# Optimization experiments

Hardware: AMD Instinct MI355X
Metric: run time of the kernel (lower is better)

Reference implementation:

```python
import jax, jax.numpy as jnp
import numpy as np

H = 16      # heads
D = 64      # head_dim
C = 64      # k_centroid
HID = H * D
TAU1 = 1.0
TAU2 = 1.0


def setup_inputs() -> dict:
    key = jax.random.key(0)
    ks = jax.random.split(key, 12)
    B, S = 4, 1024
    inv = 1.0 / np.sqrt(D)
    return {
        "query": jax.random.normal(ks[0], (B, S, HID), dtype=jnp.float32),
        "key": jax.random.normal(ks[1], (B, S, HID), dtype=jnp.float32),
        "value": jax.random.normal(ks[2], (B, S, HID), dtype=jnp.float32),
        "Wq": jax.random.uniform(ks[3], (D, D), jnp.float32, -inv, inv),
        "bq": jax.random.uniform(ks[4], (D,), jnp.float32, -inv, inv),
        "Wk": jax.random.uniform(ks[5], (D, D), jnp.float32, -inv, inv),
        "bk": jax.random.uniform(ks[6], (D,), jnp.float32, -inv, inv),
        "Wv": jax.random.uniform(ks[7], (D, D), jnp.float32, -inv, inv),
        "bv": jax.random.uniform(ks[8], (D,), jnp.float32, -inv, inv),
        "centroid": jax.random.uniform(ks[9], (D, C), jnp.float32, -0.5, 0.5),
        "Wfc": jax.random.uniform(ks[10], (HID, HID), jnp.float32, -1.0 / np.sqrt(HID), 1.0 / np.sqrt(HID)),
        "bfc": jax.random.uniform(ks[11], (HID,), jnp.float32, -1.0 / np.sqrt(HID), 1.0 / np.sqrt(HID)),
    }


def _forward(query, key, value, Wq, bq, Wk, bk, Wv, bv, centroid, Wfc, bfc):
    B, S, _ = query.shape
    q = query.reshape(B, S, H, D)
    k = key.reshape(B, S, H, D)
    v = value.reshape(B, S, H, D)
    # per-head linear projections (applied on last dim, nn.Linear equivalent)
    Q = jnp.einsum('nshd,de->nshe', q, Wq) + bq
    K = jnp.einsum('nshd,de->nshe', k, Wk) + bk
    V = jnp.einsum('nshd,de->nshe', v, Wv) + bv
    # VQ-style key quantization: project keys onto centroids, gumbel-softmax over codebook
    K_ = jnp.einsum('nshd,dc->nshc', K, centroid)            # [B,S,H,C]
    g1 = jax.random.gumbel(jax.random.key(42), K_.shape, dtype=K_.dtype)
    prob = jax.nn.softmax((K_ + g1) / TAU1, axis=-1)
    sto_K = jnp.einsum('nshc,dc->nshd', prob, centroid)      # prob @ centroid.T
    # gumbel-softmax attention over QK^T
    scores = jnp.einsum('nqhd,nkhd->nhqk', Q, sto_K)         # [B,H,S,S]
    g2 = jax.random.gumbel(jax.random.key(43), scores.shape, dtype=scores.dtype)
    attn = jax.nn.softmax((scores + g2) / TAU2, axis=3)
    out = jnp.einsum('nhql,nlhd->nqhd', attn, V).reshape(B, S, HID)
    return jnp.einsum('nsd,de->nse', out, Wfc) + bfc


def reference(query, key, value, Wq, bq, Wk, bk, Wv, bv, centroid, Wfc, bfc):
    return _forward(query, key, value, Wq, bq, Wk, bk, Wv, bv, centroid, Wfc, bfc)
```

## Files before the change

### kernel.cpp

```cpp
#include <hip/hip_runtime.h>
#include <hip/hip_bf16.h>
#include <cstdint>

typedef unsigned short u16;
typedef __attribute__((ext_vector_type(8))) short short8;
typedef __attribute__((ext_vector_type(4))) float f32x4;

#define LT 72
#define LOG2E 1.4426950408889634f

__device__ __forceinline__ u16 f2bf(float x) {
  __hip_bfloat16 h = __float2bfloat16(x);
  union { __hip_bfloat16 h; u16 u; } cv; cv.h = h; return cv.u;
}
__device__ __forceinline__ u16 f2bf_fast(float x) {
  uint32_t b = __float_as_uint(x);
  return (u16)((b + 0x7fffu + ((b >> 16) & 1u)) >> 16);
}
__device__ __forceinline__ float bf2f(u16 u) {
  union { u16 u; __hip_bfloat16 h; } cv; cv.u = u; return __bfloat162float(cv.h);
}
__device__ __forceinline__ float ld(const void* base, size_t i, int isb) {
  return isb ? bf2f(((const u16*)base)[i]) : ((const float*)base)[i];
}
__device__ __forceinline__ void st_out(void* base, size_t i, float v, int isb) {
  if (isb) ((u16*)base)[i] = f2bf_fast(v);
  else     ((float*)base)[i] = v;
}
__device__ __forceinline__ int probe_is_bf16(const void* q) {
  const u16* u = (const u16*)q;
  int sane = 0;
  for (int i = 0; i < 64; i++) {
    u16 x = u[2 * i];
    int e = (x >> 7) & 0xff;
    sane += (int)(((e >= 117) && (e <= 133)) || ((x & 0x7fff) == 0));
  }
  return sane >= 32;
}

__device__ __forceinline__ uint32_t rotl32(uint32_t x, int n) {
  return __builtin_amdgcn_alignbit(x, x, (uint32_t)(32 - n));
}
__device__ __forceinline__ void threefry4x(uint32_t k1, uint32_t x1base,
                                           uint32_t out[4]) {
  const uint32_t ks2 = k1 ^ 0x1BD11BDAu;
  uint32_t x0[4], x1[4];
  #pragma unroll
  for (int j = 0; j < 4; j++) { x0[j] = 0u; x1[j] = x1base + ((uint32_t)j << 4); }
#define R4(rot) \
  _Pragma("unroll") \
  for (int j = 0; j < 4; j++) { \
    x0[j] += x1[j]; x1[j] = rotl32(x1[j], rot); x1[j] ^= x0[j]; \
  }
  R4(13) R4(15) R4(26) R4(6)
  #pragma unroll
  for (int j = 0; j < 4; j++) { x0[j] += k1; x1[j] += ks2 + 1u; }
  R4(17) R4(29) R4(16) R4(24)
  #pragma unroll
  for (int j = 0; j < 4; j++) { x0[j] += ks2; x1[j] += 2u; }
  R4(13) R4(15) R4(26) R4(6)
  #pragma unroll
  for (int j = 0; j < 4; j++) { x1[j] += k1 + 3u; }
  R4(17) R4(29) R4(16) R4(24)
  #pragma unroll
  for (int j = 0; j < 4; j++) { x0[j] += k1; x1[j] += ks2 + 4u; }
  R4(13) R4(15) R4(26) R4(6)
  #pragma unroll
  for (int j = 0; j < 4; j++) { out[j] = (x0[j] + ks2) ^ (x1[j] + 5u); }
#undef R4
}
__device__ __forceinline__ float rcp_l2n(uint32_t bits) {
  float u = __uint_as_float(0x3f800000u | (bits >> 9)) - 1.0f;
  float l2n = -__log2f(u);
  float t = 1.0f - u;
  float fix = fmaf(0.5f * t, t, t) * LOG2E;
  l2n = (bits >= 0xFF000000u) ? fix : l2n;
  return __builtin_amdgcn_rcpf(l2n);
}
__device__ __forceinline__ float qsum(float v) {
  v += __shfl_xor(v, 1, 64);
  v += __shfl_xor(v, 2, 64);
  v += __shfl_xor(v, 4, 64);
  v += __shfl_xor(v, 8, 64);
  return v;
}
__device__ __forceinline__ void stage_tile(u16* dst, const u16* src,
                                           int src_stride, int tid) {
  #pragma unroll
  for (int i = 0; i < 2; i++) {
    int u = tid + (i << 8);
    int r = u >> 3, c8 = (u & 7) * 8;
    *(short8*)&dst[r * LT + c8] =
        *(const short8*)&src[(size_t)r * src_stride + c8];
  }
}
__device__ __forceinline__ void pf_tile(short8 regs[2], const u16* src,
                                        int src_stride, int tid) {
  #pragma unroll
  for (int i = 0; i < 2; i++) {
    int u = tid + (i << 8);
    int r = u >> 3, c8 = (u & 7) * 8;
    regs[i] = *(const short8*)&src[(size_t)r * src_stride + c8];
  }
}
__device__ __forceinline__ void flush_tile(u16* dst, const short8 regs[2],
                                           int tid) {
  #pragma unroll
  for (int i = 0; i < 2; i++) {
    int u = tid + (i << 8);
    int r = u >> 3, c8 = (u & 7) * 8;
    *(short8*)&dst[r * LT + c8] = regs[i];
  }
}
__device__ __forceinline__ void stage_x(u16* dst, const void* src, size_t base,
                                        int isb, int tid) {
  if (isb) {
    const u16* s = (const u16*)src;
    #pragma unroll
    for (int i = 0; i < 2; i++) {
      int u = tid + (i << 8);
      int r = u >> 3, c8 = (u & 7) * 8;
      *(short8*)&dst[r * LT + c8] =
          *(const short8*)&s[base + (size_t)r * 1024 + c8];
    }
  } else {
    const float* s = (const float*)src;
    #pragma unroll
    for (int i = 0; i < 4; i++) {
      int f = (tid + (i << 8)) << 2;
      int r = f >> 6, c = f & 63;
      float4 v = *(const float4*)&s[base + (size_t)r * 1024 + c];
      ushort4 w4 = {f2bf_fast(v.x), f2bf_fast(v.y), f2bf_fast(v.z),
                    f2bf_fast(v.w)};
      *(ushort4*)&dst[r * LT + c] = w4;
    }
  }
}
__device__ __forceinline__ void gemm16(const u16* A, const u16* Bt, int w,
                                       int qd, int n, f32x4 acc[4]) {
  short8 a0 = *(const short8*)&A[(16 * w + n) * LT + qd * 8];
  short8 a1 = *(const short8*)&A[(16 * w + n) * LT + qd * 8 + 32];
  #pragma unroll
  for (int ct = 0; ct < 4; ct++) {
    short8 b0 = *(const short8*)&Bt[(16 * ct + n) * LT + qd * 8];
    short8 b1 = *(const short8*)&Bt[(16 * ct + n) * LT + qd * 8 + 32];
    acc[ct] = __builtin_amdgcn_mfma_f32_16x16x32_bf16(a0, b0, acc[ct], 0, 0, 0);
    acc[ct] = __builtin_amdgcn_mfma_f32_16x16x32_bf16(a1, b1, acc[ct], 0, 0, 0);
  }
}

__global__ __launch_bounds__(256, 4) void prep_kernel(
    const void* query, const void* Wq, const void* Wk, const void* Wv,
    const void* cen, const void* Wfc,
    const void* bq, const void* bk, const void* bv, const void* bfc,
    u16* WqT, u16* WkT, u16* WvT, u16* cenT, u16* cenN, u16* WfcT,
    float* biasF, int* flagp) {
  __shared__ __align__(16) u16 T[64 * LT];
  __shared__ int sflag;
  int tid = threadIdx.x, bid = blockIdx.x;
  if (tid == 0) sflag = probe_is_bf16(query);
  __syncthreads();
  int isb = sflag;

  if (bid < 256) {
    int k0 = (bid >> 4) * 64, c0 = (bid & 15) * 64;
    if (isb) {
      const u16* s = (const u16*)Wfc;
      #pragma unroll
      for (int i = 0; i < 2; i++) {
        int u = tid + (i << 8);
        int r = u >> 3, c8 = (u & 7) * 8;
        short8 v = *(const short8*)&s[(size_t)(k0 + r) * 1024 + c0 + c8];
        #pragma unroll
        for (int e = 0; e < 8; e++) T[(c8 + e) * LT + r] = (u16)v[e];
      }
    } else {
      const float* s = (const float*)Wfc;
      #pragma unroll
      for (int i = 0; i < 4; i++) {
        int f = (tid + (i << 8)) << 2;
        int r = f >> 6, c = f & 63;
        float4 v = *(const float4*)&s[(size_t)(k0 + r) * 1024 + c0 + c];
        T[(c + 0) * LT + r] = f2bf(v.x);
        T[(c + 1) * LT + r] = f2bf(v.y);
        T[(c + 2) * LT + r] = f2bf(v.z);
        T[(c + 3) * LT + r] = f2bf(v.w);
      }
    }
    __syncthreads();
    #pragma unroll
    for (int i = 0; i < 2; i++) {
      int u = tid + (i << 8);
      int cr = u >> 3, k8 = (u & 7) * 8;
      *(short8*)&WfcT[(size_t)(c0 + cr) * 1024 + k0 + k8] =
          *(const short8*)&T[cr * LT + k8];
    }
  } else if (bid < 259) {
    const void* W = (bid == 256) ? Wq : ((bid == 257) ? Wk : Wv);
    u16* WT = (bid == 256) ? WqT : ((bid == 257) ? WkT : WvT);
    float scl = (bid == 256) ? LOG2E : 1.0f;
    #pragma unroll
    for (int i = 0; i < 16; i++) {
      int f = tid + (i << 8);
      int r = f >> 6, c = f & 63;
      T[c * LT + r] = f2bf(ld(W, f, isb) * scl);
    }
    __syncthreads();
    #pragma unroll
    for (int i = 0; i < 16; i++) {
      int f = tid + (i << 8);
      WT[f] = T[(f >> 6) * LT + (f & 63)];
    }
  } else if (bid == 259) {
    #pragma unroll
    for (int i = 0; i < 16; i++) {
      int f = tid + (i << 8);
      int d = f >> 6, c = f & 63;
      float v = ld(cen, f, isb);
      cenN[f] = f2bf(v);
      T[c * LT + d] = f2bf(v * LOG2E);
    }
    __syncthreads();
    #pragma unroll
    for (int i = 0; i < 16; i++) {
      int f = tid + (i << 8);
      cenT[f] = T[(f >> 6) * LT + (f & 63)];
    }
  } else {
    if (tid < 64) {
      biasF[tid] = ld(bq, tid, isb) * LOG2E;
      biasF[64 + tid] = ld(bk, tid, isb);
      biasF[128 + tid] = ld(bv, tid, isb);
    }
    #pragma unroll
    for (int j = 0; j < 4; j++) {
      int c = tid + (j << 8);
      biasF[192 + c] = ld(bfc, c, isb);
    }
    if (tid == 0) *flagp = isb;
  }
}

__global__ __launch_bounds__(256, 4) void proj_kernel(
    const void* q_in, const void* k_in, const void* v_in,
    const u16* WqT, const u16* WkT, const u16* WvT,
    const u16* cenT, const u16* cenN, const float* biasF, const int* flagp,
    u16* Qbf, u16* Kbf, u16* VTbf) {
  __shared__ __align__(16) u16 XB[64 * LT], WB[64 * LT], CT[64 * LT], CN[64 * LT];
  int tid = threadIdx.x;
  int w = tid >> 6, ln = tid & 63, qd = ln >> 4, n = ln & 15;
  int bh = blockIdx.x >> 4, st = blockIdx.x & 15;
  int b = bh >> 4, h = bh & 15, s0 = st * 64;
  int isb = *flagp;
  size_t xbase = ((size_t)(b * 1024 + s0)) * 1024 + h * 64;
  size_t obase = (size_t)bh * 65536 + (size_t)s0 * 64;
  f32x4 z = {0.f, 0.f, 0.f, 0.f};

  stage_tile(CT, cenT, 64, tid);
  stage_tile(CN, cenN, 64, tid);
  stage_tile(WB, WqT, 64, tid);
  stage_x(XB, q_in, xbase, isb, tid);
  __syncthreads();

  {
    f32x4 acc[4] = {z, z, z, z};
    gemm16(XB, WB, w, qd, n, acc);
    #pragma unroll
    for (int ct = 0; ct < 4; ct++) {
      int col = 16 * ct + n;
      float bia = biasF[col];
      #pragma unroll
      for (int i = 0; i < 4; i++) {
        int srow = 16 * w + 4 * qd + i;
        Qbf[obase + (size_t)srow * 64 + col] = f2bf_fast(acc[ct][i] + bia);
      }
    }
  }
  __syncthreads();
  stage_tile(WB, WkT, 64, tid);
  stage_x(XB, k_in, xbase, isb, tid);
  __syncthreads();

  {
    f32x4 acc[4] = {z, z, z, z};
    gemm16(XB, WB, w, qd, n, acc);
    #pragma unroll
    for (int ct = 0; ct < 4; ct++) {
      int col = 16 * ct + n;
      float bia = biasF[64 + col];
      #pragma unroll
      for (int i = 0; i < 4; i++)
        XB[(16 * w + 4 * qd + i) * LT + col] = f2bf_fast(acc[ct][i] + bia);
    }
    f32x4 kc[4] = {z, z, z, z};
    gemm16(XB, CT, w, qd, n, kc);
    __syncthreads();
    uint32_t idxb42 = (((((uint32_t)b << 10) |
                         (uint32_t)(s0 + 16 * w + 4 * qd)) << 10) |
                       ((uint32_t)h << 6) | (uint32_t)n) + 42u;
    float lsum[4];
    #pragma unroll
    for (int i = 0; i < 4; i++) {
      uint32_t r[4];
      threefry4x(42u, idxb42 + ((uint32_t)i << 10), r);
      float ps = 0.f;
      #pragma unroll
      for (int ct = 0; ct < 4; ct++) {
        float pv = __builtin_amdgcn_exp2f(kc[ct][i]) * rcp_l2n(r[ct]);
        ps += pv;
        WB[(16 * w + 4 * qd + i) * LT + 16 * ct + n] = f2bf_fast(pv);
      }
      lsum[i] = qsum(ps);
    }
    f32x4 sk[4] = {z, z, z, z};
    gemm16(WB, CN, w, qd, n, sk);
    #pragma unroll
    for (int i = 0; i < 4; i++) {
      float inv = __builtin_amdgcn_rcpf(lsum[i]);
      int srow = 16 * w + 4 * qd + i;
      #pragma unroll
      for (int ct = 0; ct < 4; ct++)
        Kbf[obase + (size_t)srow * 64 + 16 * ct + n] =
            f2bf_fast(sk[ct][i] * inv);
    }
  }
  __syncthreads();
  stage_tile(WB, WvT, 64, tid);
  stage_x(XB, v_in, xbase, isb, tid);
  __syncthreads();

  {
    f32x4 acc[4] = {z, z, z, z};
    gemm16(XB, WB, w, qd, n, acc);
    #pragma unroll
    for (int ct = 0; ct < 4; ct++) {
      int col = 16 * ct + n;
      float bia = biasF[128 + col];
      #pragma unroll
      for (int i = 0; i < 4; i++)
        CT[col * LT + 16 * w + 4 * qd + i] = f2bf_fast(acc[ct][i] + bia);
    }
    __syncthreads();
    #pragma unroll
    for (int i = 0; i < 2; i++) {
      int u = tid + (i << 8);
      int dr = u >> 3, c8 = (u & 7) * 8;
      *(short8*)&VTbf[(size_t)bh * 65536 + (size_t)dr * 1024 + s0 + c8] =
          *(const short8*)&CT[dr * LT + c8];
    }
  }
}

__global__ __launch_bounds__(256, 8) void gumbel_kernel(
    float* __restrict__ rnlws) {
  int tid = threadIdx.x;
  int w = tid >> 6, ln = tid & 63, qd = ln >> 4, n = ln & 15;
  int bid2 = blockIdx.x;
  int orig = bid2 >> 2, lt0 = (bid2 & 3) << 2;
  int xcd = orig & 7, m = orig >> 3;
  int bh = xcd + 8 * (m >> 4), qt = m & 15;
  int q0 = qt * 64;
  uint32_t idxb43 = (((uint32_t)bh << 20) |
                     ((uint32_t)(q0 + 16 * w + 4 * qd) << 10) | (uint32_t)n) +
                    43u;
  float* base = rnlws + (((size_t)orig * 16 + lt0) * 256 + tid) * 16;
  #pragma unroll
  for (int t = 0; t < 4; t++) {
    uint32_t base43 = idxb43 + ((uint32_t)(lt0 + t) << 6);
    #pragma unroll
    for (int i = 0; i < 4; i++) {
      uint32_t r[4];
      threefry4x(43u, base43 + ((uint32_t)i << 10), r);
      float4 v;
      v.x = rcp_l2n(r[0]); v.y = rcp_l2n(r[1]);
      v.z = rcp_l2n(r[2]); v.w = rcp_l2n(r[3]);
      *(float4*)(base + (size_t)t * 4096 + i * 4) = v;
    }
  }
}

__global__ __launch_bounds__(256, 4) void attn_pre_kernel(
    const u16* __restrict__ Qbf, const u16* __restrict__ Kbf,
    const u16* __restrict__ VTbf, const float* __restrict__ rnlws,
    u16* __restrict__ AObf) {
  __shared__ __align__(16) u16 QS[64 * LT], KS[64 * LT], VS[64 * LT], PS[64 * LT];
  int tid = threadIdx.x;
  int w = tid >> 6, ln = tid & 63, qd = ln >> 4, n = ln & 15;
  int bid = blockIdx.x;
  int xcd = bid & 7, m = bid >> 3;
  int bh = xcd + 8 * (m >> 4), qt = m & 15;
  int b = bh >> 4, h = bh & 15, q0 = qt * 64;
  f32x4 z = {0.f, 0.f, 0.f, 0.f};
  const u16* Kb = Kbf + (size_t)bh * 65536;
  const u16* Vb = VTbf + (size_t)bh * 65536;

  stage_tile(QS, Qbf + (size_t)bh * 65536 + (size_t)q0 * 64, 64, tid);

  f32x4 o[4] = {z, z, z, z};
  float lsum[4] = {0.f, 0.f, 0.f, 0.f};

  const float* rnlb = rnlws + ((size_t)bid * 16 * 256 + tid) * 16;
  float4 rc[4], rn[4];
  #pragma unroll
  for (int i = 0; i < 4; i++) rc[i] = *(const float4*)(rnlb + i * 4);

  short8 kreg[2], vreg[2];
  pf_tile(kreg, Kb, 64, tid);
  pf_tile(vreg, Vb, 1024, tid);

  for (int lt = 0; lt < 16; lt++) {
    __syncthreads();
    flush_tile(KS, kreg, tid);
    flush_tile(VS, vreg, tid);
    if (lt < 15) {
      pf_tile(kreg, Kb + (size_t)(lt + 1) * 4096, 64, tid);
      pf_tile(vreg, Vb + (lt + 1) * 64, 1024, tid);
      const float* rp = rnlb + (size_t)(lt + 1) * 4096;
      #pragma unroll
      for (int i = 0; i < 4; i++) rn[i] = *(const float4*)(rp + i * 4);
    }
    __syncthreads();

    f32x4 sc[4] = {z, z, z, z};
    gemm16(QS, KS, w, qd, n, sc);

    #pragma unroll
    for (int i = 0; i < 4; i++) {
      float r0 = (i == 0) ? rc[0].x : ((i == 1) ? rc[1].x : ((i == 2) ? rc[2].x : rc[3].x));
      float r1 = (i == 0) ? rc[0].y : ((i == 1) ? rc[1].y : ((i == 2) ? rc[2].y : rc[3].y));
      float r2 = (i == 0) ? rc[0].z : ((i == 1) ? rc[1].z : ((i == 2) ? rc[2].z : rc[3].z));
      float r3 = (i == 0) ? rc[0].w : ((i == 1) ? rc[1].w : ((i == 2) ? rc[2].w : rc[3].w));
      float rr[4] = {r0, r1, r2, r3};
      #pragma unroll
      for (int ct = 0; ct < 4; ct++) {
        float p = __builtin_amdgcn_exp2f(sc[ct][i]) * rr[ct];
        lsum[i] += p;
        PS[(16 * w + 4 * qd + i) * LT + 16 * ct + n] = f2bf_fast(p);
      }
    }
    gemm16(PS, VS, w, qd, n, o);

    #pragma unroll
    for (int i = 0; i < 4; i++) rc[i] = rn[i];
  }

  #pragma unroll
  for (int i = 0; i < 4; i++) {
    float inv = __builtin_amdgcn_rcpf(qsum(lsum[i]));
    int qrow = q0 + 16 * w + 4 * qd + i;
    size_t rb = ((size_t)(b * 1024 + qrow)) * 1024 + h * 64;
    #pragma unroll
    for (int ct = 0; ct < 4; ct++)
      AObf[rb + 16 * ct + n] = f2bf_fast(o[ct][i] * inv);
  }
}

__global__ __launch_bounds__(256, 4) void attn_kernel(
    const u16* __restrict__ Qbf, const u16* __restrict__ Kbf,
    const u16* __restrict__ VTbf, u16* __restrict__ AObf) {
  __shared__ __align__(16) u16 QS[64 * LT], KS[64 * LT], VS[64 * LT], PS[64 * LT];
  int tid = threadIdx.x;
  int w = tid >> 6, ln = tid & 63, qd = ln >> 4, n = ln & 15;
  int bid = blockIdx.x;
  int xcd = bid & 7, m = bid >> 3;
  int bh = xcd + 8 * (m >> 4), qt = m & 15;
  int b = bh >> 4, h = bh & 15, q0 = qt * 64;
  f32x4 z = {0.f, 0.f, 0.f, 0.f};
  const u16* Kb = Kbf + (size_t)bh * 65536;
  const u16* Vb = VTbf + (size_t)bh * 65536;

  stage_tile(QS, Qbf + (size_t)bh * 65536 + (size_t)q0 * 64, 64, tid);

  f32x4 o[4] = {z, z, z, z};
  float lsum[4] = {0.f, 0.f, 0.f, 0.f};
  uint32_t idxb43 = (((uint32_t)bh << 20) |
                     ((uint32_t)(q0 + 16 * w + 4 * qd) << 10) | (uint32_t)n) +
                    43u;

  short8 kreg[2], vreg[2];
  pf_tile(kreg, Kb, 64, tid);
  pf_tile(vreg, Vb, 1024, tid);

  for (int lt = 0; lt < 16; lt++) {
    float rnl[4][4];
    uint32_t base43 = idxb43 + ((uint32_t)lt << 6);
    #pragma unroll
    for (int i = 0; i < 4; i++) {
      uint32_t r[4];
      threefry4x(43u, base43 + ((uint32_t)i << 10), r);
      #pragma unroll
      for (int ct = 0; ct < 4; ct++) rnl[i][ct] = rcp_l2n(r[ct]);
    }

    __syncthreads();
    flush_tile(KS, kreg, tid);
    flush_tile(VS, vreg, tid);
    if (lt < 15) {
      pf_tile(kreg, Kb + (size_t)(lt + 1) * 4096, 64, tid);
      pf_tile(vreg, Vb + (lt + 1) * 64, 1024, tid);
    }
    __syncthreads();

    f32x4 sc[4] = {z, z, z, z};
    gemm16(QS, KS, w, qd, n, sc);

    #pragma unroll
    for (int i = 0; i < 4; i++) {
      #pragma unroll
      for (int ct = 0; ct < 4; ct++) {
        float p = __builtin_amdgcn_exp2f(sc[ct][i]) * rnl[i][ct];
        lsum[i] += p;
        PS[(16 * w + 4 * qd + i) * LT + 16 * ct + n] = f2bf_fast(p);
      }
    }
    gemm16(PS, VS, w, qd, n, o);
  }

  #pragma unroll
  for (int i = 0; i < 4; i++) {
    float inv = __builtin_amdgcn_rcpf(qsum(lsum[i]));
    int qrow = q0 + 16 * w + 4 * qd + i;
    size_t rb = ((size_t)(b * 1024 + qrow)) * 1024 + h * 64;
    #pragma unroll
    for (int ct = 0; ct < 4; ct++)
      AObf[rb + 16 * ct + n] = f2bf_fast(o[ct][i] * inv);
  }
}

__global__ __launch_bounds__(256, 4) void fc_kernel(
    const u16* __restrict__ AObf, const u16* __restrict__ WfcT,
    const float* __restrict__ biasF, const int* flagp, void* __restrict__ out) {
  __shared__ __align__(16) u16 AS[64 * LT], WS[64 * LT];
  int tid = threadIdx.x;
  int w = tid >> 6, ln = tid & 63, qd = ln >> 4, n = ln & 15;
  int r0 = (blockIdx.x >> 4) * 64, c0 = (blockIdx.x & 15) * 64;
  int isb = *flagp;
  f32x4 z = {0.f, 0.f, 0.f, 0.f};
  f32x4 acc[4] = {z, z, z, z};
  const u16* Ab = AObf + (size_t)r0 * 1024;
  const u16* Wb = WfcT + (size_t)c0 * 1024;

  short8 areg[2], wreg[2];
  pf_tile(areg, Ab, 1024, tid);
  pf_tile(wreg, Wb, 1024, tid);

  for (int kt = 0; kt < 16; kt++) {
    __syncthreads();
    flush_tile(AS, areg, tid);
    flush_tile(WS, wreg, tid);
    if (kt < 15) {
      pf_tile(areg, Ab + (kt + 1) * 64, 1024, tid);
      pf_tile(wreg, Wb + (kt + 1) * 64, 1024, tid);
    }
    __syncthreads();
    gemm16(AS, WS, w, qd, n, acc);
  }
  const float* bfcF = biasF + 192;
  #pragma unroll
  for (int ct = 0; ct < 4; ct++) {
    int col = c0 + 16 * ct + n;
    float bia = bfcF[col];
    #pragma unroll
    for (int i = 0; i < 4; i++) {
      int row = r0 + 16 * w + 4 * qd + i;
      st_out(out, (size_t)row * 1024 + col, acc[ct][i] + bia, isb);
    }
  }
}

extern "C" void kernel_launch(void* const* d_in, const int* in_sizes, int n_in,
                              void* d_out, int out_size, void* d_ws,
                              size_t ws_size, hipStream_t stream) {
  (void)in_sizes; (void)n_in; (void)out_size;
  const void* query = d_in[0];
  const void* key   = d_in[1];
  const void* value = d_in[2];
  const void* Wq = d_in[3]; const void* bq = d_in[4];
  const void* Wk = d_in[5]; const void* bk = d_in[6];
  const void* Wv = d_in[7]; const void* bv = d_in[8];
  const void* cen = d_in[9];
  const void* Wfc = d_in[10]; const void* bfc = d_in[11];

  u16* ws = (u16*)d_ws;
  u16* Qbf  = ws;
  u16* Kbf  = Qbf + 4194304;
  u16* VTbf = Kbf + 4194304;
  u16* AObf = VTbf + 4194304;
  u16* WfcT = AObf + 4194304;
  u16* WqTp = WfcT + 1048576;
  u16* WkTp = WqTp + 4096;
  u16* WvTp = WkTp + 4096;
  u16* cenTp = WvTp + 4096;
  u16* cenNp = cenTp + 4096;
  float* biasF = (float*)(cenNp + 4096);
  int* flagp = (int*)(biasF + 1216);

  const size_t RNL_OFF = 35697664ull;
  const size_t RNL_BYTES = 268435456ull;
  int use_pre = (ws_size >= RNL_OFF + RNL_BYTES);
  float* rnlws = (float*)((char*)d_ws + RNL_OFF);

  prep_kernel<<<261, 256, 0, stream>>>(query, Wq, Wk, Wv, cen, Wfc, bq, bk, bv,
                                       bfc, WqTp, WkTp, WvTp, cenTp, cenNp,
                                       WfcT, biasF, flagp);
  proj_kernel<<<1024, 256, 0, stream>>>(query, key, value, WqTp, WkTp, WvTp,
                                        cenTp, cenNp, biasF, flagp,
                                        Qbf, Kbf, VTbf);
  if (use_pre) {
    gumbel_kernel<<<4096, 256, 0, stream>>>(rnlws);
    attn_pre_kernel<<<1024, 256, 0, stream>>>(Qbf, Kbf, VTbf, rnlws, AObf);
  } else {
    attn_kernel<<<1024, 256, 0, stream>>>(Qbf, Kbf, VTbf, AObf);
  }
  fc_kernel<<<1024, 256, 0, stream>>>(AObf, WfcT, biasF, flagp, d_out);
}
```

Before: 304.3 us.

## Fuse gumbel noise generation into projection kernel and store noise as bf16

The separate gumbel kernel is removed and its work runs as extra blocks (ids 1024 and up) of the projection kernel, so the compute-bound RNG overlaps the memory-bound projection work. The precomputed noise multipliers are now stored as bf16 instead of fp32, which halves the workspace traffic for writing and re-reading them in the attention kernel. The cost is a precision loss in the noise factor, which perturbs the softmax weights slightly, and a larger single grid.

```diff
diff --git a/kernel.cpp b/kernel.cpp
--- a/kernel.cpp
+++ b/kernel.cpp
@@ -245,10 +245,36 @@
     const void* q_in, const void* k_in, const void* v_in,
     const u16* WqT, const u16* WkT, const u16* WvT,
     const u16* cenT, const u16* cenN, const float* biasF, const int* flagp,
-    u16* Qbf, u16* Kbf, u16* VTbf) {
+    u16* Qbf, u16* Kbf, u16* VTbf, u16* rnl16) {
   __shared__ __align__(16) u16 XB[64 * LT], WB[64 * LT], CT[64 * LT], CN[64 * LT];
   int tid = threadIdx.x;
   int w = tid >> 6, ln = tid & 63, qd = ln >> 4, n = ln & 15;
+
+  if (blockIdx.x >= 1024) {
+    int bid2 = blockIdx.x - 1024;
+    int orig = bid2 >> 2, lt0 = (bid2 & 3) << 2;
+    int xcd = orig & 7, mm = orig >> 3;
+    int bh = xcd + 8 * (mm >> 4), qt = mm & 15;
+    int q0 = qt * 64;
+    uint32_t idxb43 = (((uint32_t)bh << 20) |
+                       ((uint32_t)(q0 + 16 * w + 4 * qd) << 10) |
+                       (uint32_t)n) + 43u;
+    u16* gb = rnl16 + (((size_t)orig * 16 + lt0) * 256 + tid) * 16;
+    #pragma unroll
+    for (int t = 0; t < 4; t++) {
+      uint32_t b43 = idxb43 + ((uint32_t)(lt0 + t) << 6);
+      #pragma unroll
+      for (int i = 0; i < 4; i++) {
+        uint32_t r[4];
+        threefry4x(43u, b43 + ((uint32_t)i << 10), r);
+        ushort4 v = {f2bf_fast(rcp_l2n(r[0])), f2bf_fast(rcp_l2n(r[1])),
+                     f2bf_fast(rcp_l2n(r[2])), f2bf_fast(rcp_l2n(r[3]))};
+        *(ushort4*)(gb + (size_t)t * 4096 + i * 4) = v;
+      }
+    }
+    return;
+  }
+
   int bh = blockIdx.x >> 4, st = blockIdx.x & 15;
   int b = bh >> 4, h = bh & 15, s0 = st * 64;
   int isb = *flagp;
@@ -351,37 +377,9 @@
   }
 }
 
-__global__ __launch_bounds__(256, 8) void gumbel_kernel(
-    float* __restrict__ rnlws) {
-  int tid = threadIdx.x;
-  int w = tid >> 6, ln = tid & 63, qd = ln >> 4, n = ln & 15;
-  int bid2 = blockIdx.x;
-  int orig = bid2 >> 2, lt0 = (bid2 & 3) << 2;
-  int xcd = orig & 7, m = orig >> 3;
-  int bh = xcd + 8 * (m >> 4), qt = m & 15;
-  int q0 = qt * 64;
-  uint32_t idxb43 = (((uint32_t)bh << 20) |
-                     ((uint32_t)(q0 + 16 * w + 4 * qd) << 10) | (uint32_t)n) +
-                    43u;
-  float* base = rnlws + (((size_t)orig * 16 + lt0) * 256 + tid) * 16;
-  #pragma unroll
-  for (int t = 0; t < 4; t++) {
-    uint32_t base43 = idxb43 + ((uint32_t)(lt0 + t) << 6);
-    #pragma unroll
-    for (int i = 0; i < 4; i++) {
-      uint32_t r[4];
-      threefry4x(43u, base43 + ((uint32_t)i << 10), r);
-      float4 v;
-      v.x = rcp_l2n(r[0]); v.y = rcp_l2n(r[1]);
-      v.z = rcp_l2n(r[2]); v.w = rcp_l2n(r[3]);
-      *(float4*)(base + (size_t)t * 4096 + i * 4) = v;
-    }
-  }
-}
-
 __global__ __launch_bounds__(256, 4) void attn_pre_kernel(
     const u16* __restrict__ Qbf, const u16* __restrict__ Kbf,
-    const u16* __restrict__ VTbf, const float* __restrict__ rnlws,
+    const u16* __restrict__ VTbf, const u16* __restrict__ rnl16,
     u16* __restrict__ AObf) {
   __shared__ __align__(16) u16 QS[64 * LT], KS[64 * LT], VS[64 * LT], PS[64 * LT];
   int tid = threadIdx.x;
@@ -399,10 +397,10 @@
   f32x4 o[4] = {z, z, z, z};
   float lsum[4] = {0.f, 0.f, 0.f, 0.f};
 
-  const float* rnlb = rnlws + ((size_t)bid * 16 * 256 + tid) * 16;
-  float4 rc[4], rn[4];
-  #pragma unroll
-  for (int i = 0; i < 4; i++) rc[i] = *(const float4*)(rnlb + i * 4);
+  const u16* rnlb = rnl16 + (size_t)bid * 65536 + (size_t)tid * 16;
+  short8 rc0 = *(const short8*)&rnlb[0];
+  short8 rc1 = *(const short8*)&rnlb[8];
+  short8 rn0, rn1;
 
   short8 kreg[2], vreg[2];
   pf_tile(kreg, Kb, 64, tid);
@@ -415,9 +413,9 @@
     if (lt < 15) {
       pf_tile(kreg, Kb + (size_t)(lt + 1) * 4096, 64, tid);
       pf_tile(vreg, Vb + (lt + 1) * 64, 1024, tid);
-      const float* rp = rnlb + (size_t)(lt + 1) * 4096;
-      #pragma unroll
-      for (int i = 0; i < 4; i++) rn[i] = *(const float4*)(rp + i * 4);
+      const u16* rp = rnlb + (size_t)(lt + 1) * 4096;
+      rn0 = *(const short8*)&rp[0];
+      rn1 = *(const short8*)&rp[8];
     }
     __syncthreads();
 
@@ -426,22 +424,17 @@
 
     #pragma unroll
     for (int i = 0; i < 4; i++) {
-      float r0 = (i == 0) ? rc[0].x : ((i == 1) ? rc[1].x : ((i == 2) ? rc[2].x : rc[3].x));
-      float r1 = (i == 0) ? rc[0].y : ((i == 1) ? rc[1].y : ((i == 2) ? rc[2].y : rc[3].y));
-      float r2 = (i == 0) ? rc[0].z : ((i == 1) ? rc[1].z : ((i == 2) ? rc[2].z : rc[3].z));
-      float r3 = (i == 0) ? rc[0].w : ((i == 1) ? rc[1].w : ((i == 2) ? rc[2].w : rc[3].w));
-      float rr[4] = {r0, r1, r2, r3};
       #pragma unroll
       for (int ct = 0; ct < 4; ct++) {
-        float p = __builtin_amdgcn_exp2f(sc[ct][i]) * rr[ct];
+        float rr = bf2f((u16)((i < 2) ? rc0[4 * i + ct] : rc1[4 * (i - 2) + ct]));
+        float p = __builtin_amdgcn_exp2f(sc[ct][i]) * rr;
         lsum[i] += p;
         PS[(16 * w + 4 * qd + i) * LT + 16 * ct + n] = f2bf_fast(p);
       }
     }
     gemm16(PS, VS, w, qd, n, o);
 
-    #pragma unroll
-    for (int i = 0; i < 4; i++) rc[i] = rn[i];
+    rc0 = rn0; rc1 = rn1;
   }
 
   #pragma unroll
@@ -596,19 +589,18 @@
   int* flagp = (int*)(biasF + 1216);
 
   const size_t RNL_OFF = 35697664ull;
-  const size_t RNL_BYTES = 268435456ull;
+  const size_t RNL_BYTES = 134217728ull;
   int use_pre = (ws_size >= RNL_OFF + RNL_BYTES);
-  float* rnlws = (float*)((char*)d_ws + RNL_OFF);
+  u16* rnl16 = (u16*)((char*)d_ws + RNL_OFF);
 
   prep_kernel<<<261, 256, 0, stream>>>(query, Wq, Wk, Wv, cen, Wfc, bq, bk, bv,
                                        bfc, WqTp, WkTp, WvTp, cenTp, cenNp,
                                        WfcT, biasF, flagp);
-  proj_kernel<<<1024, 256, 0, stream>>>(query, key, value, WqTp, WkTp, WvTp,
-                                        cenTp, cenNp, biasF, flagp,
-                                        Qbf, Kbf, VTbf);
+  proj_kernel<<<use_pre ? 5120 : 1024, 256, 0, stream>>>(
+      query, key, value, WqTp, WkTp, WvTp, cenTp, cenNp, biasF, flagp,
+      Qbf, Kbf, VTbf, rnl16);
   if (use_pre) {
-    gumbel_kernel<<<4096, 256, 0, stream>>>(rnlws);
-    attn_pre_kernel<<<1024, 256, 0, stream>>>(Qbf, Kbf, VTbf, rnlws, AObf);
+    attn_pre_kernel<<<1024, 256, 0, stream>>>(Qbf, Kbf, VTbf, rnl16, AObf);
   } else {
     attn_kernel<<<1024, 256, 0, stream>>>(Qbf, Kbf, VTbf, AObf);
   }
```

Result: slower. 315.9 us (+3.8%).
